# Optimization experiments

Hardware: AMD Instinct MI355X
Metric: run time of the kernel (lower is better)

The kernel has to match this reference:

```python
import jax, jax.numpy as jnp
import numpy as np

D_MODEL, D_INNER, D_STATE, D_CONV, DT_RANK = 512, 1024, 16, 4, 32
B, L = 2, 2048
EPS = 1e-5


def setup_inputs() -> dict:
    key = jax.random.key(0)
    ks = jax.random.split(key, 10)
    s = 0.02
    return {
        "x": jax.random.normal(ks[0], (B, L, D_MODEL), jnp.float32),
        "attention_mask": jnp.ones((B, L), jnp.int32),
        "norm_weight": jnp.ones((D_MODEL,), jnp.float32),
        "in_proj_w": jax.random.normal(ks[1], (2 * D_INNER, D_MODEL), jnp.float32) * s,
        "conv_w": jax.random.normal(ks[2], (D_INNER, 1, D_CONV), jnp.float32) * 0.3,
        "conv_b": jnp.zeros((D_INNER,), jnp.float32),
        "x_proj_w": jax.random.normal(ks[3], (DT_RANK + 2 * D_STATE, D_INNER), jnp.float32) * s,
        "dt_proj_w": jax.random.normal(ks[4], (D_INNER, DT_RANK), jnp.float32) * 0.1,
        "dt_proj_b": jnp.full((D_INNER,), -4.6, jnp.float32),  # softplus ~ 0.01
        "A_log": jnp.log(jnp.tile(jnp.arange(1, D_STATE + 1, dtype=jnp.float32), (D_INNER, 1))),
        "D": jnp.ones((D_INNER,), jnp.float32),
        "out_proj_w": jax.random.normal(ks[5], (D_MODEL, D_INNER), jnp.float32) * s,
    }


def _mamba_block(h, in_proj_w, conv_w, conv_b, x_proj_w, dt_proj_w, dt_proj_b, A_log, D, out_proj_w):
    # in_proj -> split into x, z  (B, L, D_INNER) each
    xz = jnp.einsum("bld,ed->ble", h, in_proj_w)
    u, z = jnp.split(xz, 2, axis=-1)
    # causal depthwise conv over time, then SiLU
    u_ncl = jnp.transpose(u, (0, 2, 1))  # (B, D_INNER, L)
    conv = jax.lax.conv_general_dilated(
        u_ncl, conv_w, window_strides=(1,), padding=[(D_CONV - 1, 0)],
        feature_group_count=D_INNER, dimension_numbers=("NCH", "OIH", "NCH"))
    u = jax.nn.silu(jnp.transpose(conv + conv_b[None, :, None], (0, 2, 1)))  # (B, L, D_INNER)
    # x_proj -> dt (low rank), Bm, Cm
    xdbc = jnp.einsum("bld,ed->ble", u, x_proj_w)
    dt_r, Bm, Cm = jnp.split(xdbc, [DT_RANK, DT_RANK + D_STATE], axis=-1)
    dt = jax.nn.softplus(jnp.einsum("blr,dr->bld", dt_r, dt_proj_w) + dt_proj_b)  # (B,L,D_INNER)
    A = -jnp.exp(A_log)  # (D_INNER, D_STATE)

    def step(hstate, inputs):
        dt_t, B_t, C_t, u_t = inputs  # (B,Din), (B,Dst), (B,Dst), (B,Din)
        dA = jnp.exp(dt_t[..., None] * A)                      # (B, Din, Dst)
        dBu = dt_t[..., None] * B_t[:, None, :] * u_t[..., None]
        hstate = dA * hstate + dBu
        y_t = jnp.einsum("bds,bs->bd", hstate, C_t)
        return hstate, y_t

    xs = (jnp.swapaxes(dt, 0, 1), jnp.swapaxes(Bm, 0, 1), jnp.swapaxes(Cm, 0, 1), jnp.swapaxes(u, 0, 1))
    h0 = jnp.zeros((u.shape[0], D_INNER, D_STATE), u.dtype)
    _, ys = jax.lax.scan(step, h0, xs)
    y = jnp.swapaxes(ys, 0, 1) + D * u          # skip term
    y = y * jax.nn.silu(z)                      # gating
    return jnp.einsum("ble,de->bld", y, out_proj_w)


def reference(x, attention_mask, norm_weight, in_proj_w, conv_w, conv_b,
              x_proj_w, dt_proj_w, dt_proj_b, A_log, D, out_proj_w):
    # pre-norm RMSNorm
    var = jnp.mean(jnp.square(x), axis=-1, keepdims=True)
    h = x * jax.lax.rsqrt(var + EPS) * norm_weight
    mask = attention_mask[..., None].astype(h.dtype)
    h = h * mask
    h = _mamba_block(h, in_proj_w, conv_w, conv_b, x_proj_w, dt_proj_w, dt_proj_b, A_log, D, out_proj_w)
    h = h * mask
    return x + h
```

## Files before the change

kernel.cpp:

```cpp
#include <hip/hip_runtime.h>
#include <hip/hip_bf16.h>
#include <math.h>

#define D_MODEL 512
#define D_INNER 1024
#define D_STATE 16
#define DT_RANK 32
#define B_SZ 2
#define SEQ 2048
#define ROWS (B_SZ*SEQ)
#define EPSV 1e-5f
#define NCHUNK 64
#define CLEN (SEQ/NCHUNK)
#define NPAIR (B_SZ*D_INNER)
#define LOG2E 1.44269504088896f
#define N_ALL 1152

typedef short bf16x8 __attribute__((ext_vector_type(8)));
typedef float f32x4  __attribute__((ext_vector_type(4)));
typedef __hip_bfloat16 bf16_t;

static __device__ __forceinline__ float bf2f(bf16_t v) { return __bfloat162float(v); }

static __device__ __forceinline__ void xcd_swizzle(int& bx, int& by) {
    int gx = gridDim.x;
    int nwg = gx * gridDim.y;
    int flat = by * gx + bx;
    int q = nwg >> 3;
    int s = (flat & 7) * q + (flat >> 3);
    bx = s % gx; by = s / gx;
}

__global__ __launch_bounds__(256) void prep_kernel(
        const float* __restrict__ in_proj_w, const float* __restrict__ out_proj_w,
        const float* __restrict__ dt_proj_w, const float* __restrict__ x_proj_w,
        const float* __restrict__ x, const int* __restrict__ mask,
        const float* __restrict__ norm_w,
        bf16_t* __restrict__ w_in, bf16_t* __restrict__ w_out,
        bf16_t* __restrict__ W_all, bf16_t* __restrict__ h) {
    int bid = blockIdx.x;
    int tid = threadIdx.x;
    if (bid < 1536) {
        const float* src = (bid < 1024) ? in_proj_w : out_proj_w;
        bf16_t* dst = (bid < 1024) ? w_in : w_out;
        int i = ((bid < 1024) ? bid : (bid - 1024)) * 256 + tid;
        float4 v = reinterpret_cast<const float4*>(src)[i];
        bf16_t o[4] = {__float2bfloat16(v.x), __float2bfloat16(v.y),
                       __float2bfloat16(v.z), __float2bfloat16(v.w)};
        reinterpret_cast<ushort4*>(dst)[i] = *reinterpret_cast<ushort4*>(o);
    } else if (bid < 1792) {
        __shared__ float a[64][33];
        __shared__ float b[32][68];
        int blk = bid - 1536;
        int n0 = (blk >> 4) * 64;
        int k0 = (blk & 15) * 64;
        #pragma unroll
        for (int hh = 0; hh < 2; ++hh) {
            int q = tid + hh * 256;
            int r = q >> 3, c = (q & 7) * 4;
            float4 v = *reinterpret_cast<const float4*>(dt_proj_w + (size_t)(n0 + r) * DT_RANK + c);
            a[r][c] = v.x; a[r][c + 1] = v.y; a[r][c + 2] = v.z; a[r][c + 3] = v.w;
            int r2 = q >> 4, c2 = (q & 15) * 4;
            float4 w = *reinterpret_cast<const float4*>(x_proj_w + (size_t)r2 * D_INNER + k0 + c2);
            b[r2][c2] = w.x; b[r2][c2 + 1] = w.y; b[r2][c2 + 2] = w.z; b[r2][c2 + 3] = w.w;
        }
        __syncthreads();
        int ty = tid >> 4, tx = tid & 15;
        float acc[4][4] = {};
        #pragma unroll
        for (int r = 0; r < 32; ++r) {
            float av[4], bv[4];
            #pragma unroll
            for (int i = 0; i < 4; ++i) av[i] = a[ty * 4 + i][r];
            #pragma unroll
            for (int j = 0; j < 4; ++j) bv[j] = b[r][tx * 4 + j];
            #pragma unroll
            for (int i = 0; i < 4; ++i)
                #pragma unroll
                for (int j = 0; j < 4; ++j)
                    acc[i][j] = fmaf(av[i], bv[j], acc[i][j]);
        }
        #pragma unroll
        for (int i = 0; i < 4; ++i) {
            bf16_t o[4];
            #pragma unroll
            for (int j = 0; j < 4; ++j) o[j] = __float2bfloat16(acc[i][j]);
            *reinterpret_cast<ushort4*>(W_all + (size_t)(n0 + ty * 4 + i) * D_INNER + k0 + tx * 4) =
                *reinterpret_cast<ushort4*>(o);
        }
    } else if (bid < 1920) {
        int row = bid - 1792;
        int cq = tid * 4;
        bf16_t o[4] = {};
        if (row < 32) {
            float4 v = *reinterpret_cast<const float4*>(x_proj_w + (size_t)(32 + row) * D_INNER + cq);
            o[0] = __float2bfloat16(v.x); o[1] = __float2bfloat16(v.y);
            o[2] = __float2bfloat16(v.z); o[3] = __float2bfloat16(v.w);
        }
        *reinterpret_cast<ushort4*>(W_all + (size_t)(1024 + row) * D_INNER + cq) =
            *reinterpret_cast<ushort4*>(o);
    } else {
        __shared__ float red[4];
        int row = bid - 1920;
        const float2 v = reinterpret_cast<const float2*>(x + (size_t)row * D_MODEL)[tid];
        float ss = v.x * v.x + v.y * v.y;
        #pragma unroll
        for (int m = 1; m < 64; m <<= 1) ss += __shfl_xor(ss, m);
        if ((tid & 63) == 0) red[tid >> 6] = ss;
        __syncthreads();
        float tot = red[0] + red[1] + red[2] + red[3];
        float scale = rsqrtf(tot * (1.0f / D_MODEL) + EPSV) * (float)mask[row];
        __hip_bfloat162 o;
        o.x = __float2bfloat16(v.x * scale * norm_w[2 * tid]);
        o.y = __float2bfloat16(v.y * scale * norm_w[2 * tid + 1]);
        reinterpret_cast<__hip_bfloat162*>(h + (size_t)row * D_MODEL)[tid] = o;
    }
}

template<int MODE, int TN>
__global__ __launch_bounds__(256) void gemm_mfma(
        const bf16_t* __restrict__ A, const bf16_t* __restrict__ Bw,
        void* __restrict__ Cv, int M, int N, int K,
        const float* __restrict__ xres, const int* __restrict__ mask2,
        void* __restrict__ z2, const float* __restrict__ bias) {
    constexpr int MI  = (TN == 128) ? 4 : 2;
    constexpr int BCH = TN / 32;
    __shared__ alignas(16) bf16_t As[2][128 * 64];
    __shared__ alignas(16) bf16_t Bs[2][TN * 64];
    const int tid = threadIdx.x;
    const int wid = tid >> 6, lane = tid & 63;
    int bx = blockIdx.x, by = blockIdx.y;
    xcd_swizzle(bx, by);
    const int m0 = by * 128, n0 = bx * TN;
    const int wr = (TN == 128) ? ((wid >> 1) * 64) : (wid * 32);
    const int wc = (TN == 128) ? ((wid & 1) * 64) : 0;

    f32x4 acc[MI][4];
    #pragma unroll
    for (int i = 0; i < MI; ++i)
        #pragma unroll
        for (int j = 0; j < 4; ++j)
            #pragma unroll
            for (int r = 0; r < 4; ++r) acc[i][j][r] = 0.f;

    const int rrow = lane & 15, kg = lane >> 4;
    const int lrow = lane >> 3;
    const int cbs = (lane & 7) ^ lrow;

    auto stage = [&](bf16_t* AS, bf16_t* BS, int koff) {
        #pragma unroll
        for (int j = 0; j < 4; ++j) {
            int c = wid * 4 + j;
            int r = c * 8 + lrow;
            const bf16_t* ga = A + (size_t)(m0 + r) * K + koff + cbs * 8;
            __builtin_amdgcn_global_load_lds(
                (const __attribute__((address_space(1))) void*)ga,
                (__attribute__((address_space(3))) void*)(AS + c * 512), 16, 0, 0);
        }
        #pragma unroll
        for (int j = 0; j < BCH; ++j) {
            int c = wid * BCH + j;
            int r = c * 8 + lrow;
            const bf16_t* gb = Bw + (size_t)(n0 + r) * K + koff + cbs * 8;
            __builtin_amdgcn_global_load_lds(
                (const __attribute__((address_space(1))) void*)gb,
                (__attribute__((address_space(3))) void*)(BS + c * 512), 16, 0, 0);
        }
    };
    auto compute = [&](const bf16_t* AS, const bf16_t* BS) {
        #pragma unroll
        for (int kk = 0; kk < 2; ++kk) {
            bf16x8 af[MI], bfr[4];
            int g = kk * 4 + kg;
            #pragma unroll
            for (int i = 0; i < MI; ++i) {
                int ra = wr + i * 16 + rrow;
                af[i] = *reinterpret_cast<const bf16x8*>(AS + ra * 64 + ((g ^ (ra & 7)) * 8));
            }
            #pragma unroll
            for (int j = 0; j < 4; ++j) {
                int rb = wc + j * 16 + rrow;
                bfr[j] = *reinterpret_cast<const bf16x8*>(BS + rb * 64 + ((g ^ (rb & 7)) * 8));
            }
            #pragma unroll
            for (int i = 0; i < MI; ++i)
                #pragma unroll
                for (int j = 0; j < 4; ++j)
                    acc[i][j] = __builtin_amdgcn_mfma_f32_16x16x32_bf16(af[i], bfr[j], acc[i][j], 0, 0, 0);
        }
    };

    stage(As[0], Bs[0], 0);
    __syncthreads();
    for (int k0 = 0; k0 < K; k0 += 128) {
        stage(As[1], Bs[1], k0 + 64);
        compute(As[0], Bs[0]);
        __syncthreads();
        if (k0 + 128 < K) stage(As[0], Bs[0], k0 + 128);
        compute(As[1], Bs[1]);
        __syncthreads();
    }

    #pragma unroll
    for (int i = 0; i < MI; ++i)
        #pragma unroll
        for (int j = 0; j < 4; ++j)
            #pragma unroll
            for (int rg = 0; rg < 4; ++rg) {
                int m = m0 + wr + i * 16 + (lane >> 4) * 4 + rg;
                int n = n0 + wc + j * 16 + (lane & 15);
                float v = acc[i][j][rg];
                if (MODE == 2) {
                    ((float*)Cv)[(size_t)m * N + n] = xres[(size_t)m * N + n] + (float)mask2[m] * v;
                } else if (MODE == 3) {
                    if (n < D_INNER)
                        ((bf16_t*)Cv)[(size_t)m * D_INNER + n] = __float2bfloat16(v);
                    else
                        ((bf16_t*)z2)[(size_t)m * D_INNER + (n - D_INNER)] = __float2bfloat16(v);
                } else {
                    if (n < D_INNER) {
                        float s = v + bias[n];
                        s = (s > 20.f) ? s : __logf(1.f + __expf(s));
                        ((bf16_t*)Cv)[(size_t)m * D_INNER + n] = __float2bfloat16(s);
                    } else if (n < D_INNER + 32) {
                        ((float*)z2)[(size_t)m * 32 + (n - D_INNER)] = v;
                    }
                }
            }
}

__global__ __launch_bounds__(256) void conv_silu_kernel(const bf16_t* __restrict__ upre,
        const float* __restrict__ conv_w, const float* __restrict__ conv_b,
        bf16_t* __restrict__ u) {
    int idx = blockIdx.x * 256 + threadIdx.x;
    int dp = idx & 511;
    int row = idx >> 9;
    int t = row & (SEQ - 1);
    const __hip_bfloat162* base =
        reinterpret_cast<const __hip_bfloat162*>(upre + (size_t)(row - t) * D_INNER) + dp;
    int d0 = 2 * dp;
    float sx = conv_b[d0], sy = conv_b[d0 + 1];
    #pragma unroll
    for (int j = 0; j < 4; ++j) {
        int tt = t - 3 + j;
        if (tt >= 0) {
            __hip_bfloat162 vv = base[(size_t)tt * 512];
            sx = fmaf(conv_w[d0 * 4 + j], bf2f(vv.x), sx);
            sy = fmaf(conv_w[(d0 + 1) * 4 + j], bf2f(vv.y), sy);
        }
    }
    __hip_bfloat162 o;
    o.x = __float2bfloat16(sx / (1.f + __expf(-sx)));
    o.y = __float2bfloat16(sy / (1.f + __expf(-sy)));
    reinterpret_cast<__hip_bfloat162*>(u)[idx] = o;
}

__global__ __launch_bounds__(256) void scan_phase1(
        const bf16_t* __restrict__ dtb, const bf16_t* __restrict__ ub,
        const float* __restrict__ bcbuf, const float* __restrict__ A_log,
        float* __restrict__ P, float* __restrict__ F) {
    int tid = threadIdx.x;
    int bid = blockIdx.x;
    int dblk = bid & 3, c = (bid >> 2) & (NCHUNK - 1), b = bid >> 8;
    int d = dblk * 256 + tid;
    __shared__ float sBC[CLEN][32];
    size_t rb = (size_t)b * SEQ + (size_t)c * CLEN;
    {
        int row = tid >> 3, q = tid & 7;
        *reinterpret_cast<float4*>(&sBC[row][q * 4]) =
            *reinterpret_cast<const float4*>(bcbuf + (rb + row) * 32 + q * 4);
    }
    float A2[16];
    #pragma unroll
    for (int s4 = 0; s4 < 4; ++s4) {
        float4 a = *reinterpret_cast<const float4*>(A_log + d * D_STATE + s4 * 4);
        A2[s4 * 4 + 0] = -expf(a.x) * LOG2E;
        A2[s4 * 4 + 1] = -expf(a.y) * LOG2E;
        A2[s4 * 4 + 2] = -expf(a.z) * LOG2E;
        A2[s4 * 4 + 3] = -expf(a.w) * LOG2E;
    }
    float p[16], f[16];
    #pragma unroll
    for (int s = 0; s < 16; ++s) { p[s] = 1.f; f[s] = 0.f; }
    const bf16_t* dtp = dtb + rb * D_INNER + d;
    const bf16_t* up  = ub  + rb * D_INNER + d;
    float dtc[4], uc[4];
    #pragma unroll
    for (int j = 0; j < 4; ++j) {
        dtc[j] = bf2f(dtp[(size_t)j * D_INNER]);
        uc[j]  = bf2f(up[(size_t)j * D_INNER]);
    }
    __syncthreads();
    for (int tb = 0; tb < CLEN; tb += 4) {
        float dtn[4], un[4];
        if (tb + 4 < CLEN) {
            #pragma unroll
            for (int j = 0; j < 4; ++j) {
                dtn[j] = bf2f(dtp[(size_t)(tb + 4 + j) * D_INNER]);
                un[j]  = bf2f(up[(size_t)(tb + 4 + j) * D_INNER]);
            }
        } else {
            #pragma unroll
            for (int j = 0; j < 4; ++j) { dtn[j] = 0.f; un[j] = 0.f; }
        }
        #pragma unroll
        for (int j = 0; j < 4; ++j) {
            float dtv = dtc[j];
            float dtu = dtv * uc[j];
            #pragma unroll
            for (int s = 0; s < 16; ++s) {
                float e = exp2f(dtv * A2[s]);
                p[s] *= e;
                f[s] = fmaf(e, f[s], sBC[tb + j][s] * dtu);
            }
        }
        #pragma unroll
        for (int j = 0; j < 4; ++j) { dtc[j] = dtn[j]; uc[j] = un[j]; }
    }
    size_t o = ((size_t)(b * D_INNER + d) * NCHUNK + c) * D_STATE;
    #pragma unroll
    for (int s4 = 0; s4 < 4; ++s4) {
        float4 vp = {p[s4*4+0], p[s4*4+1], p[s4*4+2], p[s4*4+3]};
        float4 vf = {f[s4*4+0], f[s4*4+1], f[s4*4+2], f[s4*4+3]};
        *reinterpret_cast<float4*>(P + o + s4 * 4) = vp;
        *reinterpret_cast<float4*>(F + o + s4 * 4) = vf;
    }
}

__global__ __launch_bounds__(256) void scan_phase2(
        float* __restrict__ P, const float* __restrict__ F) {
    int idx = blockIdx.x * 256 + threadIdx.x;
    int pair = idx >> 4, s = idx & 15;
    size_t base = (size_t)pair * NCHUNK * D_STATE + s;
    float pp[8], ff[8];
    #pragma unroll
    for (int j = 0; j < 8; ++j) {
        pp[j] = P[base + (size_t)j * D_STATE];
        ff[j] = F[base + (size_t)j * D_STATE];
    }
    float h = 0.f;
    #pragma unroll
    for (int cb = 0; cb < 8; ++cb) {
        #pragma unroll
        for (int j = 0; j < 8; ++j) {
            int c = cb * 8 + j;
            float p = pp[j], f = ff[j];
            if (cb < 7) {
                pp[j] = P[base + (size_t)(c + 8) * D_STATE];
                ff[j] = F[base + (size_t)(c + 8) * D_STATE];
            }
            P[base + (size_t)c * D_STATE] = h;
            h = fmaf(p, h, f);
        }
    }
}

__global__ __launch_bounds__(256) void scan_phase3(
        const bf16_t* __restrict__ dtb, const bf16_t* __restrict__ ub,
        const float* __restrict__ bcbuf, const bf16_t* __restrict__ zbuf,
        const float* __restrict__ A_log, const float* __restrict__ Dw,
        const float* __restrict__ Hinit, bf16_t* __restrict__ ybuf) {
    int tid = threadIdx.x;
    int bid = blockIdx.x;
    int dblk = bid & 3, c = (bid >> 2) & (NCHUNK - 1), b = bid >> 8;
    int d = dblk * 256 + tid;
    __shared__ float sBC[CLEN][32];
    size_t rb = (size_t)b * SEQ + (size_t)c * CLEN;
    {
        int row = tid >> 3, q = tid & 7;
        *reinterpret_cast<float4*>(&sBC[row][q * 4]) =
            *reinterpret_cast<const float4*>(bcbuf + (rb + row) * 32 + q * 4);
    }
    float A2[16];
    #pragma unroll
    for (int s4 = 0; s4 < 4; ++s4) {
        float4 a = *reinterpret_cast<const float4*>(A_log + d * D_STATE + s4 * 4);
        A2[s4 * 4 + 0] = -expf(a.x) * LOG2E;
        A2[s4 * 4 + 1] = -expf(a.y) * LOG2E;
        A2[s4 * 4 + 2] = -expf(a.z) * LOG2E;
        A2[s4 * 4 + 3] = -expf(a.w) * LOG2E;
    }
    float Dd = Dw[d];
    float st[16];
    size_t o = ((size_t)(b * D_INNER + d) * NCHUNK + c) * D_STATE;
    #pragma unroll
    for (int s4 = 0; s4 < 4; ++s4) {
        float4 hv = *reinterpret_cast<const float4*>(Hinit + o + s4 * 4);
        st[s4*4+0] = hv.x; st[s4*4+1] = hv.y; st[s4*4+2] = hv.z; st[s4*4+3] = hv.w;
    }
    const bf16_t* dtp = dtb + rb * D_INNER + d;
    const bf16_t* up  = ub  + rb * D_INNER + d;
    const bf16_t* zp  = zbuf + rb * D_INNER + d;
    bf16_t* yp = ybuf + rb * D_INNER + d;
    float dtc[4], uc[4], zc[4];
    #pragma unroll
    for (int j = 0; j < 4; ++j) {
        dtc[j] = bf2f(dtp[(size_t)j * D_INNER]);
        uc[j]  = bf2f(up[(size_t)j * D_INNER]);
        zc[j]  = bf2f(zp[(size_t)j * D_INNER]);
    }
    __syncthreads();
    for (int tb = 0; tb < CLEN; tb += 4) {
        float dtn[4], un[4], zn[4];
        if (tb + 4 < CLEN) {
            #pragma unroll
            for (int j = 0; j < 4; ++j) {
                dtn[j] = bf2f(dtp[(size_t)(tb + 4 + j) * D_INNER]);
                un[j]  = bf2f(up[(size_t)(tb + 4 + j) * D_INNER]);
                zn[j]  = bf2f(zp[(size_t)(tb + 4 + j) * D_INNER]);
            }
        } else {
            #pragma unroll
            for (int j = 0; j < 4; ++j) { dtn[j] = 0.f; un[j] = 0.f; zn[j] = 0.f; }
        }
        #pragma unroll
        for (int j = 0; j < 4; ++j) {
            float dtv = dtc[j];
            float dtu = dtv * uc[j];
            float y = 0.f;
            #pragma unroll
            for (int s = 0; s < 16; ++s) {
                float e = exp2f(dtv * A2[s]);
                st[s] = fmaf(e, st[s], sBC[tb + j][s] * dtu);
                y = fmaf(st[s], sBC[tb + j][16 + s], y);
            }
            float zv = zc[j];
            float sig = 1.f / (1.f + __expf(-zv));
            yp[(size_t)(tb + j) * D_INNER] = __float2bfloat16((y + Dd * uc[j]) * (zv * sig));
        }
        #pragma unroll
        for (int j = 0; j < 4; ++j) { dtc[j] = dtn[j]; uc[j] = un[j]; zc[j] = zn[j]; }
    }
}

extern "C" void kernel_launch(void* const* d_in, const int* in_sizes, int n_in,
                              void* d_out, int out_size, void* d_ws, size_t ws_size,
                              hipStream_t stream) {
    const float* x          = (const float*)d_in[0];
    const int*   mask       = (const int*)d_in[1];
    const float* norm_w     = (const float*)d_in[2];
    const float* in_proj_w  = (const float*)d_in[3];
    const float* conv_w     = (const float*)d_in[4];
    const float* conv_b     = (const float*)d_in[5];
    const float* x_proj_w   = (const float*)d_in[6];
    const float* dt_proj_w  = (const float*)d_in[7];
    const float* dt_proj_b  = (const float*)d_in[8];
    const float* A_log      = (const float*)d_in[9];
    const float* Dw         = (const float*)d_in[10];
    const float* out_proj_w = (const float*)d_in[11];
    float* out = (float*)d_out;
    float* ws  = (float*)d_ws;

    bf16_t* u_pre = (bf16_t*)ws;
    bf16_t* zbuf  = (bf16_t*)(ws + 2097152);
    bf16_t* u_bf  = (bf16_t*)(ws + 6291456);
    bf16_t* dt_bf = (bf16_t*)(ws + 8388608);
    bf16_t* h_bf  = (bf16_t*)(ws + 10485760);
    bf16_t* y_bf  = (bf16_t*)(ws + 10485760);
    float*  bcbuf = ws + 12582912;
    float*  Pbuf  = ws + 12845056;
    bf16_t* w_in  = (bf16_t*)(ws + 12845056);
    float*  Fbuf  = ws + 14942208;
    bf16_t* W_all = (bf16_t*)(ws + 14942208);
    bf16_t* w_out = (bf16_t*)(ws + 17039360);

    prep_kernel<<<6016, 256, 0, stream>>>(in_proj_w, out_proj_w, dt_proj_w, x_proj_w,
                                          x, mask, norm_w, w_in, w_out, W_all, h_bf);
    gemm_mfma<3, 128><<<dim3(16, 32), 256, 0, stream>>>(
        h_bf, w_in, u_pre, ROWS, 2 * D_INNER, D_MODEL, nullptr, nullptr, zbuf, nullptr);
    conv_silu_kernel<<<(ROWS * D_INNER / 2) / 256, 256, 0, stream>>>(u_pre, conv_w, conv_b, u_bf);
    gemm_mfma<4, 128><<<dim3(N_ALL / 128, 32), 256, 0, stream>>>(
        u_bf, W_all, dt_bf, ROWS, N_ALL, D_INNER, nullptr, nullptr, bcbuf, dt_proj_b);
    scan_phase1<<<B_SZ * NCHUNK * 4, 256, 0, stream>>>(dt_bf, u_bf, bcbuf, A_log, Pbuf, Fbuf);
    scan_phase2<<<NPAIR * D_STATE / 256, 256, 0, stream>>>(Pbuf, Fbuf);
    scan_phase3<<<B_SZ * NCHUNK * 4, 256, 0, stream>>>(dt_bf, u_bf, bcbuf, zbuf, A_log, Dw,
                                                       Pbuf, y_bf);
    gemm_mfma<2, 64><<<dim3(8, 32), 256, 0, stream>>>(
        y_bf, w_out, out, ROWS, D_MODEL, D_INNER, x, mask, nullptr, nullptr);
}
```

Baseline: 181.3 us.

## Split scan state across thread pairs and vectorize conv to 8-wide loads

The chunked scan phases now give each channel two threads, each holding 8 of the 16 states. The partial y values are combined with a lane shuffle, and twice as many blocks are launched to raise occupancy and cut per-thread serial work. The depthwise conv+SiLU kernel now processes 8 channels per thread using 128-bit bf16 loads and stores instead of 2-wide accesses. This costs duplicated dt/u/z loads per channel pair and some idle lanes at the y store.

```diff
diff --git a/kernel.cpp b/kernel.cpp
--- a/kernel.cpp
+++ b/kernel.cpp
@@ -21,6 +21,9 @@
 typedef __hip_bfloat16 bf16_t;
 
 static __device__ __forceinline__ float bf2f(bf16_t v) { return __bfloat162float(v); }
+static __device__ __forceinline__ float bfraw2f(short v) {
+    return __uint_as_float(((unsigned)(unsigned short)v) << 16);
+}
 
 static __device__ __forceinline__ void xcd_swizzle(int& bx, int& by) {
     int gx = gridDim.x;
@@ -233,26 +236,36 @@
         const float* __restrict__ conv_w, const float* __restrict__ conv_b,
         bf16_t* __restrict__ u) {
     int idx = blockIdx.x * 256 + threadIdx.x;
-    int dp = idx & 511;
-    int row = idx >> 9;
+    int dq = idx & 127;
+    int row = idx >> 7;
     int t = row & (SEQ - 1);
-    const __hip_bfloat162* base =
-        reinterpret_cast<const __hip_bfloat162*>(upre + (size_t)(row - t) * D_INNER) + dp;
-    int d0 = 2 * dp;
-    float sx = conv_b[d0], sy = conv_b[d0 + 1];
+    int d0 = dq * 8;
+    const bf16_t* base = upre + (size_t)(row - t) * D_INNER + d0;
+    float s_[8];
+    {
+        float4 b0 = *reinterpret_cast<const float4*>(conv_b + d0);
+        float4 b1 = *reinterpret_cast<const float4*>(conv_b + d0 + 4);
+        s_[0] = b0.x; s_[1] = b0.y; s_[2] = b0.z; s_[3] = b0.w;
+        s_[4] = b1.x; s_[5] = b1.y; s_[6] = b1.z; s_[7] = b1.w;
+    }
     #pragma unroll
     for (int j = 0; j < 4; ++j) {
         int tt = t - 3 + j;
         if (tt >= 0) {
-            __hip_bfloat162 vv = base[(size_t)tt * 512];
-            sx = fmaf(conv_w[d0 * 4 + j], bf2f(vv.x), sx);
-            sy = fmaf(conv_w[(d0 + 1) * 4 + j], bf2f(vv.y), sy);
-        }
-    }
-    __hip_bfloat162 o;
-    o.x = __float2bfloat16(sx / (1.f + __expf(-sx)));
-    o.y = __float2bfloat16(sy / (1.f + __expf(-sy)));
-    reinterpret_cast<__hip_bfloat162*>(u)[idx] = o;
+            bf16x8 vv = *reinterpret_cast<const bf16x8*>(base + (size_t)tt * D_INNER);
+            #pragma unroll
+            for (int i = 0; i < 8; ++i)
+                s_[i] = fmaf(conv_w[(d0 + i) * 4 + j], bfraw2f(vv[i]), s_[i]);
+        }
+    }
+    bf16_t o[8];
+    #pragma unroll
+    for (int i = 0; i < 8; ++i) {
+        float v = s_[i];
+        o[i] = __float2bfloat16(v / (1.f + __expf(-v)));
+    }
+    *reinterpret_cast<bf16x8*>(u + (size_t)row * D_INNER + d0) =
+        *reinterpret_cast<bf16x8*>(o);
 }
 
 __global__ __launch_bounds__(256) void scan_phase1(
@@ -261,8 +274,9 @@
         float* __restrict__ P, float* __restrict__ F) {
     int tid = threadIdx.x;
     int bid = blockIdx.x;
-    int dblk = bid & 3, c = (bid >> 2) & (NCHUNK - 1), b = bid >> 8;
-    int d = dblk * 256 + tid;
+    int dblk = bid & 7, c = (bid >> 3) & (NCHUNK - 1), b = bid >> 9;
+    int d = dblk * 128 + (tid >> 1);
+    int sh = (tid & 1) * 8;
     __shared__ float sBC[CLEN][32];
     size_t rb = (size_t)b * SEQ + (size_t)c * CLEN;
     {
@@ -270,18 +284,18 @@
         *reinterpret_cast<float4*>(&sBC[row][q * 4]) =
             *reinterpret_cast<const float4*>(bcbuf + (rb + row) * 32 + q * 4);
     }
-    float A2[16];
-    #pragma unroll
-    for (int s4 = 0; s4 < 4; ++s4) {
-        float4 a = *reinterpret_cast<const float4*>(A_log + d * D_STATE + s4 * 4);
+    float A2[8];
+    #pragma unroll
+    for (int s4 = 0; s4 < 2; ++s4) {
+        float4 a = *reinterpret_cast<const float4*>(A_log + d * D_STATE + sh + s4 * 4);
         A2[s4 * 4 + 0] = -expf(a.x) * LOG2E;
         A2[s4 * 4 + 1] = -expf(a.y) * LOG2E;
         A2[s4 * 4 + 2] = -expf(a.z) * LOG2E;
         A2[s4 * 4 + 3] = -expf(a.w) * LOG2E;
     }
-    float p[16], f[16];
-    #pragma unroll
-    for (int s = 0; s < 16; ++s) { p[s] = 1.f; f[s] = 0.f; }
+    float p[8], f[8];
+    #pragma unroll
+    for (int s = 0; s < 8; ++s) { p[s] = 1.f; f[s] = 0.f; }
     const bf16_t* dtp = dtb + rb * D_INNER + d;
     const bf16_t* up  = ub  + rb * D_INNER + d;
     float dtc[4], uc[4];
@@ -308,18 +322,18 @@
             float dtv = dtc[j];
             float dtu = dtv * uc[j];
             #pragma unroll
-            for (int s = 0; s < 16; ++s) {
+            for (int s = 0; s < 8; ++s) {
                 float e = exp2f(dtv * A2[s]);
                 p[s] *= e;
-                f[s] = fmaf(e, f[s], sBC[tb + j][s] * dtu);
+                f[s] = fmaf(e, f[s], sBC[tb + j][sh + s] * dtu);
             }
         }
         #pragma unroll
         for (int j = 0; j < 4; ++j) { dtc[j] = dtn[j]; uc[j] = un[j]; }
     }
-    size_t o = ((size_t)(b * D_INNER + d) * NCHUNK + c) * D_STATE;
-    #pragma unroll
-    for (int s4 = 0; s4 < 4; ++s4) {
+    size_t o = ((size_t)(b * D_INNER + d) * NCHUNK + c) * D_STATE + sh;
+    #pragma unroll
+    for (int s4 = 0; s4 < 2; ++s4) {
         float4 vp = {p[s4*4+0], p[s4*4+1], p[s4*4+2], p[s4*4+3]};
         float4 vf = {f[s4*4+0], f[s4*4+1], f[s4*4+2], f[s4*4+3]};
         *reinterpret_cast<float4*>(P + o + s4 * 4) = vp;
@@ -362,8 +376,9 @@
         const float* __restrict__ Hinit, bf16_t* __restrict__ ybuf) {
     int tid = threadIdx.x;
     int bid = blockIdx.x;
-    int dblk = bid & 3, c = (bid >> 2) & (NCHUNK - 1), b = bid >> 8;
-    int d = dblk * 256 + tid;
+    int dblk = bid & 7, c = (bid >> 3) & (NCHUNK - 1), b = bid >> 9;
+    int d = dblk * 128 + (tid >> 1);
+    int sh = (tid & 1) * 8;
     __shared__ float sBC[CLEN][32];
     size_t rb = (size_t)b * SEQ + (size_t)c * CLEN;
     {
@@ -371,20 +386,20 @@
         *reinterpret_cast<float4*>(&sBC[row][q * 4]) =
             *reinterpret_cast<const float4*>(bcbuf + (rb + row) * 32 + q * 4);
     }
-    float A2[16];
-    #pragma unroll
-    for (int s4 = 0; s4 < 4; ++s4) {
-        float4 a = *reinterpret_cast<const float4*>(A_log + d * D_STATE + s4 * 4);
+    float A2[8];
+    #pragma unroll
+    for (int s4 = 0; s4 < 2; ++s4) {
+        float4 a = *reinterpret_cast<const float4*>(A_log + d * D_STATE + sh + s4 * 4);
         A2[s4 * 4 + 0] = -expf(a.x) * LOG2E;
         A2[s4 * 4 + 1] = -expf(a.y) * LOG2E;
         A2[s4 * 4 + 2] = -expf(a.z) * LOG2E;
         A2[s4 * 4 + 3] = -expf(a.w) * LOG2E;
     }
     float Dd = Dw[d];
-    float st[16];
-    size_t o = ((size_t)(b * D_INNER + d) * NCHUNK + c) * D_STATE;
-    #pragma unroll
-    for (int s4 = 0; s4 < 4; ++s4) {
+    float st[8];
+    size_t o = ((size_t)(b * D_INNER + d) * NCHUNK + c) * D_STATE + sh;
+    #pragma unroll
+    for (int s4 = 0; s4 < 2; ++s4) {
         float4 hv = *reinterpret_cast<const float4*>(Hinit + o + s4 * 4);
         st[s4*4+0] = hv.x; st[s4*4+1] = hv.y; st[s4*4+2] = hv.z; st[s4*4+3] = hv.w;
     }
@@ -419,14 +434,17 @@
             float dtu = dtv * uc[j];
             float y = 0.f;
             #pragma unroll
-            for (int s = 0; s < 16; ++s) {
+            for (int s = 0; s < 8; ++s) {
                 float e = exp2f(dtv * A2[s]);
-                st[s] = fmaf(e, st[s], sBC[tb + j][s] * dtu);
-                y = fmaf(st[s], sBC[tb + j][16 + s], y);
-            }
-            float zv = zc[j];
-            float sig = 1.f / (1.f + __expf(-zv));
-            yp[(size_t)(tb + j) * D_INNER] = __float2bfloat16((y + Dd * uc[j]) * (zv * sig));
+                st[s] = fmaf(e, st[s], sBC[tb + j][sh + s] * dtu);
+                y = fmaf(st[s], sBC[tb + j][16 + sh + s], y);
+            }
+            y += __shfl_xor(y, 1);
+            if ((tid & 1) == 0) {
+                float zv = zc[j];
+                float sig = 1.f / (1.f + __expf(-zv));
+                yp[(size_t)(tb + j) * D_INNER] = __float2bfloat16((y + Dd * uc[j]) * (zv * sig));
+            }
         }
         #pragma unroll
         for (int j = 0; j < 4; ++j) { dtc[j] = dtn[j]; uc[j] = un[j]; zc[j] = zn[j]; }
@@ -468,12 +486,12 @@
                                           x, mask, norm_w, w_in, w_out, W_all, h_bf);
     gemm_mfma<3, 128><<<dim3(16, 32), 256, 0, stream>>>(
         h_bf, w_in, u_pre, ROWS, 2 * D_INNER, D_MODEL, nullptr, nullptr, zbuf, nullptr);
-    conv_silu_kernel<<<(ROWS * D_INNER / 2) / 256, 256, 0, stream>>>(u_pre, conv_w, conv_b, u_bf);
+    conv_silu_kernel<<<(ROWS * D_INNER / 8) / 256, 256, 0, stream>>>(u_pre, conv_w, conv_b, u_bf);
     gemm_mfma<4, 128><<<dim3(N_ALL / 128, 32), 256, 0, stream>>>(
         u_bf, W_all, dt_bf, ROWS, N_ALL, D_INNER, nullptr, nullptr, bcbuf, dt_proj_b);
-    scan_phase1<<<B_SZ * NCHUNK * 4, 256, 0, stream>>>(dt_bf, u_bf, bcbuf, A_log, Pbuf, Fbuf);
+    scan_phase1<<<B_SZ * NCHUNK * 8, 256, 0, stream>>>(dt_bf, u_bf, bcbuf, A_log, Pbuf, Fbuf);
     scan_phase2<<<NPAIR * D_STATE / 256, 256, 0, stream>>>(Pbuf, Fbuf);
-    scan_phase3<<<B_SZ * NCHUNK * 4, 256, 0, stream>>>(dt_bf, u_bf, bcbuf, zbuf, A_log, Dw,
+    scan_phase3<<<B_SZ * NCHUNK * 8, 256, 0, stream>>>(dt_bf, u_bf, bcbuf, zbuf, A_log, Dw,
                                                        Pbuf, y_bf);
     gemm_mfma<2, 64><<<dim3(8, 32), 256, 0, stream>>>(
         y_bf, w_out, out, ROWS, D_MODEL, D_INNER, x, mask, nullptr, nullptr);
```

Result: faster. 175.1 us (-3.4%).
